# Performance work log

Measured on AMD Instinct MI355X. Metric: run time of the kernel, lower is better.

## Reference

```python
import jax, jax.numpy as jnp
import numpy as np

N_NODES = 10000
N_EDGES = 160000
B = 128
HEADS = 4
DIMS = [36, 128, 256, 512]
NEG_SLOPE = 0.2  # PyG GATConv default


def setup_inputs() -> dict:
    key = jax.random.key(0)
    ks = jax.random.split(key, 32)
    inp = {}
    inp["x"] = jax.random.normal(ks[0], (N_NODES, DIMS[0]), jnp.float32)
    inp["edge_index"] = jax.random.randint(ks[1], (2, N_EDGES), 0, N_NODES)
    inp["batch"] = jnp.sort(jax.random.randint(ks[2], (N_NODES,), 0, B))
    ki = 3
    for i in range(3):
        din, dout = DIMS[i], DIMS[i + 1]
        C = dout // HEADS
        inp[f"gcn_w{i}"] = jax.random.normal(ks[ki], (din, dout), jnp.float32) * (din ** -0.5); ki += 1
        inp[f"gcn_b{i}"] = jnp.zeros((dout,), jnp.float32)
        inp[f"gat_w{i}"] = jax.random.normal(ks[ki], (dout, dout), jnp.float32) * (dout ** -0.5); ki += 1
        inp[f"gat_as{i}"] = jax.random.normal(ks[ki], (HEADS, C), jnp.float32) * 0.1; ki += 1
        inp[f"gat_ad{i}"] = jax.random.normal(ks[ki], (HEADS, C), jnp.float32) * 0.1; ki += 1
        inp[f"gat_b{i}"] = jnp.zeros((dout,), jnp.float32)
    D = DIMS[-1]
    inp["ap_w1"] = jax.random.normal(ks[ki], (D, D // 2), jnp.float32) * (D ** -0.5); ki += 1
    inp["ap_b1"] = jnp.zeros((D // 2,), jnp.float32)
    inp["ap_w2"] = jax.random.normal(ks[ki], (D // 2, 1), jnp.float32) * ((D // 2) ** -0.5); ki += 1
    inp["ap_b2"] = jnp.zeros((1,), jnp.float32)
    return inp


def _gcn(x, w, b, src, dst, n):
    # PyG GCNConv: add self-loops, symmetric deg^-1/2 normalization, bias after agg
    h = x @ w  # [N, dout]
    deg = jax.ops.segment_sum(jnp.ones_like(dst, dtype=h.dtype), dst, n) + 1.0  # incl. self-loop
    dinv = deg ** -0.5
    norm = dinv[src] * dinv[dst]  # [E]
    agg = jax.ops.segment_sum(h[src] * norm[:, None], dst, n)
    agg = agg + h * (dinv * dinv)[:, None]  # self-loop messages
    return agg + b


def _gat(x, w, a_s, a_d, b, src, dst, n):
    # PyG GATConv: self-loops, leaky-relu logits, segment softmax over dst, concat heads
    C = w.shape[1] // HEADS
    h = (x @ w).reshape(n, HEADS, C)
    alpha_src = (h * a_s).sum(-1)  # [N, H]
    alpha_dst = (h * a_d).sum(-1)  # [N, H]
    loop = jnp.arange(n)
    s = jnp.concatenate([src, loop])
    d = jnp.concatenate([dst, loop])
    e = jax.nn.leaky_relu(alpha_src[s] + alpha_dst[d], NEG_SLOPE)  # [E+N, H]
    m = jax.ops.segment_max(e, d, n)
    ex = jnp.exp(e - m[d])
    den = jax.ops.segment_sum(ex, d, n)
    alpha = ex / den[d]  # [E+N, H]
    out = jax.ops.segment_sum(h[s] * alpha[:, :, None], d, n)  # [N, H, C]
    return out.reshape(n, HEADS * C) + b


def _forward(x, edge_index, batch, params, ap_w1, ap_b1, ap_w2, ap_b2):
    src, dst = edge_index[0], edge_index[1]
    n = x.shape[0]
    x_in = x
    n_layers = len(params)
    for i, (gw, gb, aw, a_s, a_d, ab) in enumerate(params):
        h = jax.nn.relu(_gcn(x, gw, gb, src, dst, n))  # dropout is identity in eval
        x = h + _gat(h, aw, a_s, a_d, ab, src, dst, n)
        if i < n_layers - 1:
            if x.shape[-1] == x_in.shape[-1]:
                x = x + x_in
            x_in = x
    # attention pooling (global softmax then per-graph masked renorm)
    a = jnp.tanh(x @ ap_w1 + ap_b1) @ ap_w2 + ap_b2  # [N, 1]
    a = jax.nn.softmax(a, axis=0)
    mask = jax.nn.one_hot(batch, B, dtype=x.dtype)  # [N, B]
    aw_ = a * mask
    aw_ = aw_ / (aw_.sum(0, keepdims=True) + 1e-8)
    graph_emb = aw_.T @ x  # [B, D]
    cnt = jax.ops.segment_sum(jnp.ones((n,), x.dtype), batch, B)
    ssum = jax.ops.segment_sum(x, batch, B)
    mean = ssum / jnp.maximum(cnt, 1.0)[:, None]
    smax = jax.ops.segment_max(x, batch, B)
    return jnp.concatenate([graph_emb, mean, smax, ssum], axis=1)  # [B, 4*D]


def reference(x, edge_index, batch,
              gcn_w0, gcn_b0, gat_w0, gat_as0, gat_ad0, gat_b0,
              gcn_w1, gcn_b1, gat_w1, gat_as1, gat_ad1, gat_b1,
              gcn_w2, gcn_b2, gat_w2, gat_as2, gat_ad2, gat_b2,
              ap_w1, ap_b1, ap_w2, ap_b2):
    params = [
        (gcn_w0, gcn_b0, gat_w0, gat_as0, gat_ad0, gat_b0),
        (gcn_w1, gcn_b1, gat_w1, gat_as1, gat_ad1, gat_b1),
        (gcn_w2, gcn_b2, gat_w2, gat_as2, gat_ad2, gat_b2),
    ]
    return _forward(x, edge_index, batch, params, ap_w1, ap_b1, ap_w2, ap_b2)
```

## Files before the change

kernel.cpp:

```cpp
#include <hip/hip_runtime.h>
#include <math.h>

#define NN 10000
#define NE 160000
#define NB 128
#define NH 4
#define DOUT 512
#define NEG 0.2f

typedef __attribute__((ext_vector_type(8))) short short8;
typedef __attribute__((ext_vector_type(4))) float f32x4;
typedef __attribute__((ext_vector_type(4))) unsigned short us4;

__device__ __forceinline__ float leakyf(float v){ return v > 0.f ? v : NEG*v; }
__device__ __forceinline__ void fma4(float4& a, const float4 v, float w){
  a.x += v.x*w; a.y += v.y*w; a.z += v.z*w; a.w += v.w*w;
}
__device__ __forceinline__ unsigned short f2bf(float f){
  unsigned int u = __float_as_uint(f);
  u += 0x7FFFu + ((u >> 16) & 1u);
  return (unsigned short)(u >> 16);
}
__device__ __forceinline__ float bf2f(unsigned short h){
  return __uint_as_float(((unsigned int)h) << 16);
}
__device__ __forceinline__ void split2(float v, unsigned short& h, unsigned short& l){
  h = f2bf(v);
  l = f2bf(v - bf2f(h));
}
__device__ __forceinline__ void store_hl(unsigned short* H, unsigned short* L,
                                         size_t base, float4 v){
  us4 h, l; unsigned short hh, ll;
  split2(v.x, hh, ll); h[0]=hh; l[0]=ll;
  split2(v.y, hh, ll); h[1]=hh; l[1]=ll;
  split2(v.z, hh, ll); h[2]=hh; l[2]=ll;
  split2(v.w, hh, ll); h[3]=hh; l[3]=ll;
  *(us4*)&H[base] = h;
  *(us4*)&L[base] = l;
}
__device__ __forceinline__ float4 load_hl(const unsigned short* __restrict__ H,
                                          const unsigned short* __restrict__ L, size_t base){
  us4 h = *(const us4*)&H[base];
  us4 l = *(const us4*)&L[base];
  return make_float4(bf2f(h[0])+bf2f(l[0]), bf2f(h[1])+bf2f(l[1]),
                     bf2f(h[2])+bf2f(l[2]), bf2f(h[3])+bf2f(l[3]));
}
__device__ __forceinline__ void gl_lds16(const unsigned short* g, unsigned short* l){
  __builtin_amdgcn_global_load_lds(
      (const __attribute__((address_space(1))) unsigned int*)g,
      (__attribute__((address_space(3))) unsigned int*)l, 16, 0, 0);
}

__global__ void k_count(const int* __restrict__ dst, int* __restrict__ cnt){
  int e = blockIdx.x*blockDim.x + threadIdx.x;
  if (e < NE) atomicAdd(&cnt[dst[e]], 1);
}
__global__ void k_scan(const int* __restrict__ cnt, int* __restrict__ rowptr,
                       float* __restrict__ dinv, int* __restrict__ cursor,
                       const int* __restrict__ batch, int* __restrict__ starts){
  __shared__ int part[256];
  const int CH = (NN + 255) / 256;
  int t = threadIdx.x;
  int base = t * CH;
  int s = 0;
  for (int i = 0; i < CH; i++){ int idx = base + i; if (idx < NN) s += cnt[idx]; }
  part[t] = s; __syncthreads();
  for (int o = 1; o < 256; o <<= 1){
    int v = 0;
    if (t >= o) v = part[t - o];
    __syncthreads();
    if (t >= o) part[t] += v;
    __syncthreads();
  }
  int pre = (t == 0) ? 0 : part[t - 1];
  for (int i = 0; i < CH; i++){
    int idx = base + i;
    if (idx < NN){
      int c = cnt[idx];
      rowptr[idx] = pre; pre += c;
      dinv[idx] = rsqrtf((float)c + 1.f);
      cursor[idx] = 0;
    }
  }
  if (t == 255) rowptr[NN] = part[255];
  if (t <= NB){
    int lo = 0, hi = NN;
    while (lo < hi){ int mid = (lo + hi) >> 1; if (batch[mid] < t) lo = mid + 1; else hi = mid; }
    starts[t] = lo;
  }
}
__global__ void k_fill(const int* __restrict__ src, const int* __restrict__ dst,
                       const int* __restrict__ rowptr, int* __restrict__ cursor,
                       int* __restrict__ colidx){
  int e = blockIdx.x*blockDim.x + threadIdx.x;
  if (e >= NE) return;
  int d = dst[e];
  int pos = atomicAdd(&cursor[d], 1);
  colidx[rowptr[d] + pos] = src[e];
}

struct AllConv {
  const float* src[8];
  unsigned short* dh[8];
  unsigned short* dl[8];
  int K[8], Mm[8], Kp[8], tot[8];
};
__global__ void k_convall(AllConv a){
  int j = blockIdx.y;
  int idx = blockIdx.x*blockDim.x + threadIdx.x;
  if (idx >= a.tot[j]) return;
  float v;
  if (j == 0){
    int n = idx >> 6, c = idx & 63;
    v = (c < 36) ? a.src[0][n*36 + c] : 0.f;
  } else {
    int Kp = a.Kp[j], K = a.K[j], M = a.Mm[j];
    int kk = idx % Kp, m = idx / Kp;
    v = (kk < K) ? a.src[j][(size_t)kk*M + m] : 0.f;
  }
  unsigned short h, l; split2(v, h, l);
  a.dh[j][idx] = h; a.dl[j][idx] = l;
}

#define GBM 64
#define GBN 128
#define GBK 32
__global__ __launch_bounds__(256) void k_gemm_bf3(
    const unsigned short* __restrict__ Ah, const unsigned short* __restrict__ Al,
    const unsigned short* __restrict__ Bh, const unsigned short* __restrict__ Bl,
    float* __restrict__ C, int N, int Kp, int M, int mode,
    const float* __restrict__ bias, unsigned short* __restrict__ outH,
    unsigned short* __restrict__ outL,
    const float* __restrict__ a_s, const float* __restrict__ a_d,
    float* __restrict__ as_o, float* __restrict__ ad_o, int Cdim){
  __shared__ unsigned short AsH[GBM*GBK], AsL[GBM*GBK];
  __shared__ unsigned short BsH[GBN*GBK], BsL[GBN*GBK];
  __shared__ float sred[2][GBM][4];
  int gx = M / GBN;
  int gy = (N + GBM - 1) / GBM;
  const int G = 8;
  int bid = blockIdx.x;
  int full = gy / G;
  int bid_full = full * G * gx;
  int by, bx;
  if (bid < bid_full){
    int g = bid / (G*gx); int rem = bid % (G*gx);
    by = g*G + rem % G; bx = rem / G;
  } else {
    int rem = bid - bid_full; int rows = gy - full*G;
    by = full*G + rem % rows; bx = rem / rows;
  }
  int row0 = by * GBM, col0 = bx * GBN;
  int t = threadIdx.x;
  int w = t >> 6, L = t & 63;
  int lm = L & 15, lq = L >> 4;
  int wc = w * 32;

  int sr = L >> 2, sc = L & 3;
  int art = w*16 + sr;
  int ga  = (sc - ((art >> 1) & 3)) & 3;
  int agrow = min(row0 + art, N-1);
  int brt0 = w*16 + sr;
  int brt1 = (w+4)*16 + sr;
  int gb0 = (sc - ((brt0 >> 1) & 3)) & 3;
  int gb1 = (sc - ((brt1 >> 1) & 3)) & 3;
  int bgrow0 = col0 + brt0, bgrow1 = col0 + brt1;

  int rc = (lq + (lm >> 1)) & 3;
  int aoff[4], boff[2];
#pragma unroll
  for (int mi = 0; mi < 4; mi++) aoff[mi] = (mi*16 + lm)*32 + rc*8;
#pragma unroll
  for (int ni = 0; ni < 2; ni++) boff[ni] = (wc + ni*16 + lm)*32 + rc*8;

  f32x4 acc[4][2];
#pragma unroll
  for (int i = 0; i < 4; i++)
#pragma unroll
    for (int j = 0; j < 2; j++) acc[i][j] = (f32x4){0.f,0.f,0.f,0.f};

  int nk = Kp / GBK;
  for (int kt = 0; kt < nk; kt++){
    int k0 = kt * GBK;
    if (kt) __syncthreads();
    gl_lds16(&Ah[(size_t)agrow*Kp + k0 + ga*8],  &AsH[w*512]);
    gl_lds16(&Al[(size_t)agrow*Kp + k0 + ga*8],  &AsL[w*512]);
    gl_lds16(&Bh[(size_t)bgrow0*Kp + k0 + gb0*8], &BsH[w*512]);
    gl_lds16(&Bh[(size_t)bgrow1*Kp + k0 + gb1*8], &BsH[(w+4)*512]);
    gl_lds16(&Bl[(size_t)bgrow0*Kp + k0 + gb0*8], &BsL[w*512]);
    gl_lds16(&Bl[(size_t)bgrow1*Kp + k0 + gb1*8], &BsL[(w+4)*512]);
    __syncthreads();

    short8 ah[4], al[4], bh[2], bl[2];
#pragma unroll
    for (int mi = 0; mi < 4; mi++){
      ah[mi] = *(const short8*)&AsH[aoff[mi]];
      al[mi] = *(const short8*)&AsL[aoff[mi]];
    }
#pragma unroll
    for (int ni = 0; ni < 2; ni++){
      bh[ni] = *(const short8*)&BsH[boff[ni]];
      bl[ni] = *(const short8*)&BsL[boff[ni]];
    }
#pragma unroll
    for (int mi = 0; mi < 4; mi++)
#pragma unroll
      for (int ni = 0; ni < 2; ni++){
        acc[mi][ni] = __builtin_amdgcn_mfma_f32_16x16x32_bf16(ah[mi], bh[ni], acc[mi][ni], 0, 0, 0);
        acc[mi][ni] = __builtin_amdgcn_mfma_f32_16x16x32_bf16(ah[mi], bl[ni], acc[mi][ni], 0, 0, 0);
        acc[mi][ni] = __builtin_amdgcn_mfma_f32_16x16x32_bf16(al[mi], bh[ni], acc[mi][ni], 0, 0, 0);
      }
  }
  if (mode == 1){
#pragma unroll
    for (int mi = 0; mi < 4; mi++)
#pragma unroll
      for (int ni = 0; ni < 2; ni++){
#pragma unroll
        for (int r = 0; r < 4; r++){
          int row = row0 + mi*16 + lq*4 + r;
          int col = col0 + wc + ni*16 + lm;
          if (row < N){
            float v = fmaxf(acc[mi][ni][r] + bias[col], 0.f);
            unsigned short hh, ll; split2(v, hh, ll);
            outH[(size_t)row*M + col] = hh;
            outL[(size_t)row*M + col] = ll;
          }
        }
      }
  } else if (mode != 3){
#pragma unroll
    for (int mi = 0; mi < 4; mi++)
#pragma unroll
      for (int ni = 0; ni < 2; ni++){
#pragma unroll
        for (int r = 0; r < 4; r++){
          int row = row0 + mi*16 + lq*4 + r;
          int col = col0 + wc + ni*16 + lm;
          if (row < N) C[(size_t)row*M + col] = acc[mi][ni][r];
        }
      }
  }
  if (mode == 2){
    float sA0 = a_s[col0 + wc + lm], sA1 = a_s[col0 + wc + 16 + lm];
    float dA0 = a_d[col0 + wc + lm], dA1 = a_d[col0 + wc + 16 + lm];
#pragma unroll
    for (int mi = 0; mi < 4; mi++)
#pragma unroll
      for (int r = 0; r < 4; r++){
        float vs = acc[mi][0][r]*sA0 + acc[mi][1][r]*sA1;
        float vd = acc[mi][0][r]*dA0 + acc[mi][1][r]*dA1;
#pragma unroll
        for (int o = 1; o <= 8; o <<= 1){
          vs += __shfl_xor(vs, o);
          vd += __shfl_xor(vd, o);
        }
        if (lm == 0){
          int row = mi*16 + lq*4 + r;
          sred[0][row][w] = vs;
          sred[1][row][w] = vd;
        }
      }
    __syncthreads();
    if (t < GBM){
      int n = row0 + t;
      if (n < N){
        int wph = Cdim >> 5;
        int nheads = 4 / wph;
        for (int g = 0; g < nheads; g++){
          float ss = 0.f, dd = 0.f;
          for (int q = 0; q < wph; q++){
            ss += sred[0][t][g*wph + q];
            dd += sred[1][t][g*wph + q];
          }
          int hd = (col0 + g*wph*32) / Cdim;
          as_o[n*NH + hd] = ss;
          ad_o[n*NH + hd] = dd;
        }
      }
    }
  } else if (mode == 3){
    float b0 = bias[col0 + wc + lm], b1v = bias[col0 + wc + 16 + lm];
    float w0v = a_s[col0 + wc + lm], w1v = a_s[col0 + wc + 16 + lm];
#pragma unroll
    for (int mi = 0; mi < 4; mi++)
#pragma unroll
      for (int r = 0; r < 4; r++){
        float v = tanhf(acc[mi][0][r] + b0)*w0v + tanhf(acc[mi][1][r] + b1v)*w1v;
#pragma unroll
        for (int o = 1; o <= 8; o <<= 1) v += __shfl_xor(v, o);
        if (lm == 0) sred[0][mi*16 + lq*4 + r][w] = v;
      }
    __syncthreads();
    if (t < GBM){
      int n = row0 + t;
      if (n < N){
        float s = sred[0][t][0] + sred[0][t][1] + sred[0][t][2] + sred[0][t][3];
        atomicAdd(&as_o[n], s);
      }
    }
  }
}

__global__ __launch_bounds__(256) void k_gcn_pre(
    const unsigned short* __restrict__ inH, const unsigned short* __restrict__ inL,
    const float* __restrict__ dinv,
    const int* __restrict__ rowptr, const int* __restrict__ colidx,
    unsigned short* __restrict__ outH, unsigned short* __restrict__ outL,
    int Kp, int nchunk){
  int bid = blockIdx.x;
  int chunk = bid % nchunk, grp = bid / nchunk;
  int t = threadIdx.x;
  int sub = t & 15;
  int n = grp*16 + (t >> 4);
  if (n >= NN) return;
  int f0 = chunk*64 + sub*4;
  int b = rowptr[n], e = rowptr[n+1];
  float dn = dinv[n];
  float4 a0 = make_float4(0,0,0,0), a1 = make_float4(0,0,0,0);
  float4 a2 = make_float4(0,0,0,0), a3 = make_float4(0,0,0,0);
  int j = b;
  for (; j + 3 < e; j += 4){
    int s0 = colidx[j], s1 = colidx[j+1], s2 = colidx[j+2], s3 = colidx[j+3];
    float w0 = dinv[s0], w1 = dinv[s1], w2 = dinv[s2], w3 = dinv[s3];
    float4 v0 = load_hl(inH, inL, (size_t)s0*Kp + f0);
    float4 v1 = load_hl(inH, inL, (size_t)s1*Kp + f0);
    float4 v2 = load_hl(inH, inL, (size_t)s2*Kp + f0);
    float4 v3 = load_hl(inH, inL, (size_t)s3*Kp + f0);
    fma4(a0, v0, w0*dn); fma4(a1, v1, w1*dn);
    fma4(a2, v2, w2*dn); fma4(a3, v3, w3*dn);
  }
  for (; j < e; j++){
    int s = colidx[j];
    float4 v = load_hl(inH, inL, (size_t)s*Kp + f0);
    fma4(a0, v, dinv[s]*dn);
  }
  float4 acc = make_float4(a0.x+a1.x+a2.x+a3.x, a0.y+a1.y+a2.y+a3.y,
                           a0.z+a1.z+a2.z+a3.z, a0.w+a1.w+a2.w+a3.w);
  float4 sv = load_hl(inH, inL, (size_t)n*Kp + f0);
  float dn2 = dn*dn;
  acc.x += sv.x*dn2; acc.y += sv.y*dn2; acc.z += sv.z*dn2; acc.w += sv.w*dn2;
  store_hl(outH, outL, (size_t)n*Kp + f0, acc);
}

__global__ void k_gat_maxden(const int* __restrict__ rowptr, const int* __restrict__ colidx,
                             const float* __restrict__ as_, const float* __restrict__ ad_,
                             float* __restrict__ eself, float* __restrict__ den,
                             float* __restrict__ mmax, float* __restrict__ ealpha){
  int idx = blockIdx.x*blockDim.x + threadIdx.x;
  if (idx >= NN*NH) return;
  int n = idx >> 2, hd = idx & 3;
  float adn = ad_[idx];
  float selflog = leakyf(as_[idx] + adn);
  int b = rowptr[n], e = rowptr[n+1];
  float m = selflog, d = 1.f;
  int j = b;
  for (; j + 3 < e; j += 4){
    int s0 = colidx[j], s1 = colidx[j+1], s2 = colidx[j+2], s3 = colidx[j+3];
    float l0 = leakyf(as_[s0*NH + hd] + adn), l1 = leakyf(as_[s1*NH + hd] + adn);
    float l2 = leakyf(as_[s2*NH + hd] + adn), l3 = leakyf(as_[s3*NH + hd] + adn);
    ealpha[(size_t)(j+0)*NH + hd] = l0; ealpha[(size_t)(j+1)*NH + hd] = l1;
    ealpha[(size_t)(j+2)*NH + hd] = l2; ealpha[(size_t)(j+3)*NH + hd] = l3;
    float m4 = fmaxf(fmaxf(l0, l1), fmaxf(l2, l3));
    if (m4 > m){ d *= expf(m - m4); m = m4; }
    d += expf(l0 - m) + expf(l1 - m) + expf(l2 - m) + expf(l3 - m);
  }
  for (; j < e; j++){
    float l = leakyf(as_[colidx[j]*NH + hd] + adn);
    ealpha[(size_t)j*NH + hd] = l;
    if (l > m){ d *= expf(m - l); m = l; }
    d += expf(l - m);
  }
  eself[idx] = expf(selflog - m);
  den[idx] = d;
  mmax[idx] = m;
}
__global__ __launch_bounds__(256) void k_gat_gather(
    const float* __restrict__ hg,
    const unsigned short* __restrict__ inH, const unsigned short* __restrict__ inL,
    const int* __restrict__ rowptr, const int* __restrict__ colidx,
    const float* __restrict__ ealpha, const float* __restrict__ eself,
    const float* __restrict__ den, const float* __restrict__ mmax,
    const float* __restrict__ ab,
    unsigned short* __restrict__ outH, unsigned short* __restrict__ outL,
    int M, int C, int nchunk){
  int bid = blockIdx.x;
  int chunk = bid % nchunk, grp = bid / nchunk;
  int t = threadIdx.x;
  int sub = t & 15;
  int n = grp*16 + (t >> 4);
  if (n >= NN) return;
  int f0 = chunk*64 + sub*4;
  int hd = f0 / C;
  int b = rowptr[n], e = rowptr[n+1];
  int ai = n*NH + hd;
  float mm = mmax[ai];
  float4 a0 = make_float4(0,0,0,0), a1 = make_float4(0,0,0,0);
  float4 a2 = make_float4(0,0,0,0), a3 = make_float4(0,0,0,0);
  int j = b;
  for (; j + 3 < e; j += 4){
    int s0 = colidx[j], s1 = colidx[j+1], s2 = colidx[j+2], s3 = colidx[j+3];
    float e0 = expf(ealpha[(size_t)(j+0)*NH + hd] - mm);
    float e1 = expf(ealpha[(size_t)(j+1)*NH + hd] - mm);
    float e2 = expf(ealpha[(size_t)(j+2)*NH + hd] - mm);
    float e3 = expf(ealpha[(size_t)(j+3)*NH + hd] - mm);
    float4 v0 = *(const float4*)&hg[(size_t)s0*M + f0];
    float4 v1 = *(const float4*)&hg[(size_t)s1*M + f0];
    float4 v2 = *(const float4*)&hg[(size_t)s2*M + f0];
    float4 v3 = *(const float4*)&hg[(size_t)s3*M + f0];
    fma4(a0, v0, e0); fma4(a1, v1, e1);
    fma4(a2, v2, e2); fma4(a3, v3, e3);
  }
  for (; j < e; j++){
    int s = colidx[j];
    float4 v = *(const float4*)&hg[(size_t)s*M + f0];
    fma4(a0, v, expf(ealpha[(size_t)j*NH + hd] - mm));
  }
  float4 acc = make_float4(a0.x+a1.x+a2.x+a3.x, a0.y+a1.y+a2.y+a3.y,
                           a0.z+a1.z+a2.z+a3.z, a0.w+a1.w+a2.w+a3.w);
  float es = eself[ai], inv = 1.f/den[ai];
  float4 sv = *(const float4*)&hg[(size_t)n*M + f0];
  float4 hv = load_hl(inH, inL, (size_t)n*M + f0);
  float4 bb = *(const float4*)&ab[f0];
  float4 r = make_float4(
    hv.x + bb.x + (sv.x*es + acc.x)*inv,
    hv.y + bb.y + (sv.y*es + acc.y)*inv,
    hv.z + bb.z + (sv.z*es + acc.z)*inv,
    hv.w + bb.w + (sv.w*es + acc.w)*inv);
  store_hl(outH, outL, (size_t)n*M + f0, r);
}

__global__ void k_pool(const unsigned short* __restrict__ xH, const unsigned short* __restrict__ xL,
                       const float* __restrict__ apre, const int* __restrict__ starts,
                       float* __restrict__ out){
  __shared__ float red[128];
  int g = blockIdx.x, t = threadIdx.x;
  int b = starts[g], e = starts[g+1];
  float m = -INFINITY;
  for (int n = b + t; n < e; n += 128) m = fmaxf(m, apre[n]);
  red[t] = m; __syncthreads();
  for (int o = 64; o > 0; o >>= 1){
    if (t < o) red[t] = fmaxf(red[t], red[t + o]);
    __syncthreads();
  }
  m = red[0]; __syncthreads();
  float s = 0.f;
  for (int n = b + t; n < e; n += 128) s += expf(apre[n] - m);
  red[t] = s; __syncthreads();
  for (int o = 64; o > 0; o >>= 1){
    if (t < o) red[t] += red[t + o];
    __syncthreads();
  }
  float inv = 1.f / (red[0] + 1e-8f);
  float4 sum = make_float4(0,0,0,0), wacc = make_float4(0,0,0,0);
  float4 mx = make_float4(-INFINITY,-INFINITY,-INFINITY,-INFINITY);
  for (int n = b; n < e; n++){
    float4 xv = load_hl(xH, xL, (size_t)n*DOUT + t*4);
    float p = expf(apre[n] - m) * inv;
    sum.x += xv.x; sum.y += xv.y; sum.z += xv.z; sum.w += xv.w;
    mx.x = fmaxf(mx.x, xv.x); mx.y = fmaxf(mx.y, xv.y);
    mx.z = fmaxf(mx.z, xv.z); mx.w = fmaxf(mx.w, xv.w);
    fma4(wacc, xv, p);
  }
  float ic = 1.f / fmaxf((float)(e - b), 1.f);
  float4* o = (float4*)(out + (size_t)g*4*DOUT);
  o[t]       = wacc;
  o[128 + t] = make_float4(sum.x*ic, sum.y*ic, sum.z*ic, sum.w*ic);
  o[256 + t] = mx;
  o[384 + t] = sum;
}

extern "C" void kernel_launch(void* const* d_in, const int* in_sizes, int n_in,
                              void* d_out, int out_size, void* d_ws, size_t ws_size,
                              hipStream_t stream) {
  const float* x0   = (const float*)d_in[0];
  const int*   ei   = (const int*)d_in[1];
  const int*   src  = ei;
  const int*   dst  = ei + NE;
  const int*   batch= (const int*)d_in[2];
  const float* gw[3]  = {(const float*)d_in[3],  (const float*)d_in[9],  (const float*)d_in[15]};
  const float* gb[3]  = {(const float*)d_in[4],  (const float*)d_in[10], (const float*)d_in[16]};
  const float* aw[3]  = {(const float*)d_in[5],  (const float*)d_in[11], (const float*)d_in[17]};
  const float* asw[3] = {(const float*)d_in[6],  (const float*)d_in[12], (const float*)d_in[18]};
  const float* adw[3] = {(const float*)d_in[7],  (const float*)d_in[13], (const float*)d_in[19]};
  const float* ab[3]  = {(const float*)d_in[8],  (const float*)d_in[14], (const float*)d_in[20]};
  const float* apw1 = (const float*)d_in[21];
  const float* apb1 = (const float*)d_in[22];
  const float* apw2 = (const float*)d_in[23];
  float* out = (float*)d_out;

  char* p = (char*)d_ws;
  auto alloc = [&](size_t bytes) -> void* {
    void* r = (void*)p; p += (bytes + 255) & ~(size_t)255; return r;
  };
  float* f1 = (float*)alloc((size_t)NN*512*4);
  unsigned short* actH0 = (unsigned short*)alloc((size_t)NN*512*2);
  unsigned short* actL0 = (unsigned short*)alloc((size_t)NN*512*2);
  unsigned short* actH1 = (unsigned short*)alloc((size_t)NN*512*2);
  unsigned short* actL1 = (unsigned short*)alloc((size_t)NN*512*2);
  unsigned short* preH  = (unsigned short*)alloc((size_t)NN*256*2);
  unsigned short* preL  = (unsigned short*)alloc((size_t)NN*256*2);
  unsigned short* x0h = (unsigned short*)alloc((size_t)NN*64*2);
  unsigned short* x0l = (unsigned short*)alloc((size_t)NN*64*2);
  const int wK[7]  = {36, 128, 128, 256, 256, 512, 512};
  const int wM[7]  = {128, 128, 256, 256, 512, 512, 256};
  const int wKp[7] = {64, 128, 128, 256, 256, 512, 512};
  const float* wsrc[7] = {gw[0], aw[0], gw[1], aw[1], gw[2], aw[2], apw1};
  unsigned short* wTh[7]; unsigned short* wTl[7];
  for (int i = 0; i < 7; i++){
    size_t sz = (size_t)wM[i]*wKp[i]*2;
    wTh[i] = (unsigned short*)alloc(sz);
    wTl[i] = (unsigned short*)alloc(sz);
  }
  float* ealpha = (float*)alloc((size_t)NE*NH*4);
  float* dinv = (float*)alloc(NN*4);
  float* as_  = (float*)alloc(NN*NH*4);
  float* ad_  = (float*)alloc(NN*NH*4);
  float* eself= (float*)alloc(NN*NH*4);
  float* den  = (float*)alloc(NN*NH*4);
  float* mmax = (float*)alloc(NN*NH*4);
  float* apre = (float*)alloc(NN*4);
  int* rowptr = (int*)alloc((NN+1)*4);
  int* colidx = (int*)alloc((size_t)NE*4);
  int* cnt    = (int*)alloc(NN*4);
  int* cursor = (int*)alloc(NN*4);
  int* starts = (int*)alloc((NB+1)*4);

  hipMemsetAsync(cnt, 0, NN*sizeof(int), stream);
  k_count<<<(NE+255)/256, 256, 0, stream>>>(dst, cnt);
  k_scan<<<1, 256, 0, stream>>>(cnt, rowptr, dinv, cursor, batch, starts);
  k_fill<<<(NE+255)/256, 256, 0, stream>>>(src, dst, rowptr, cursor, colidx);

  AllConv ac;
  ac.src[0] = x0; ac.dh[0] = x0h; ac.dl[0] = x0l;
  ac.K[0] = 36; ac.Mm[0] = NN; ac.Kp[0] = 64; ac.tot[0] = NN*64;
  int maxtot = NN*64;
  for (int i = 0; i < 7; i++){
    ac.src[i+1] = wsrc[i]; ac.dh[i+1] = wTh[i]; ac.dl[i+1] = wTl[i];
    ac.K[i+1] = wK[i]; ac.Mm[i+1] = wM[i]; ac.Kp[i+1] = wKp[i];
    ac.tot[i+1] = wKp[i]*wM[i];
    if (ac.tot[i+1] > maxtot) maxtot = ac.tot[i+1];
  }
  k_convall<<<dim3((maxtot+255)/256, 8), 256, 0, stream>>>(ac);

  const int dims[4] = {36, 128, 256, 512};
  const int ngrp = (NN + 15) / 16;
  const unsigned short* curH = x0h; const unsigned short* curL = x0l;
  int wi = 0;
  for (int i = 0; i < 3; i++){
    int Kin = (i == 0) ? 64 : dims[i];
    int M = dims[i+1], C = M/NH;
    int nchunk_in = Kin / 64;
    int nchunk = M / 64;
    int nblk = (M/GBN) * ((NN+GBM-1)/GBM);
    k_gcn_pre<<<nchunk_in*ngrp, 256, 0, stream>>>(curH, curL, dinv, rowptr, colidx,
                                                  preH, preL, Kin, nchunk_in);
    k_gemm_bf3<<<nblk, 256, 0, stream>>>(preH, preL, wTh[wi], wTl[wi], f1, NN, wKp[wi], M,
                                         1, gb[i], actH0, actL0,
                                         nullptr, nullptr, nullptr, nullptr, C);
    wi++;
    k_gemm_bf3<<<nblk, 256, 0, stream>>>(actH0, actL0, wTh[wi], wTl[wi], f1, NN, wKp[wi], M,
                                         2, nullptr, nullptr, nullptr,
                                         asw[i], adw[i], as_, ad_, C);
    wi++;
    k_gat_maxden<<<(NN*NH+255)/256, 256, 0, stream>>>(rowptr, colidx, as_, ad_,
                                                      eself, den, mmax, ealpha);
    k_gat_gather<<<nchunk*ngrp, 256, 0, stream>>>(f1, actH0, actL0, rowptr, colidx,
                                                  ealpha, eself, den, mmax, ab[i],
                                                  actH1, actL1, M, C, nchunk);
    curH = actH1; curL = actL1;
  }

  hipMemsetAsync(apre, 0, NN*sizeof(float), stream);
  {
    int nblk = (256/GBN) * ((NN+GBM-1)/GBM);
    k_gemm_bf3<<<nblk, 256, 0, stream>>>(actH1, actL1, wTh[6], wTl[6], f1, NN, wKp[6], 256,
                                         3, apb1, nullptr, nullptr,
                                         apw2, nullptr, apre, nullptr, 64);
  }
  k_pool<<<NB, 128, 0, stream>>>(actH1, actL1, apre, starts, out);
}
```

Measured before the change: 455.9 us.

## Fuse GAT softmax max/denominator into gather with online softmax

```diff
diff --git a/kernel.cpp b/kernel.cpp
--- a/kernel.cpp
+++ b/kernel.cpp
@@ -15,6 +15,9 @@
 __device__ __forceinline__ float leakyf(float v){ return v > 0.f ? v : NEG*v; }
 __device__ __forceinline__ void fma4(float4& a, const float4 v, float w){
   a.x += v.x*w; a.y += v.y*w; a.z += v.z*w; a.w += v.w*w;
+}
+__device__ __forceinline__ void mul4(float4& a, float s){
+  a.x *= s; a.y *= s; a.z *= s; a.w *= s;
 }
 __device__ __forceinline__ unsigned short f2bf(float f){
   unsigned int u = __float_as_uint(f);
@@ -57,7 +60,8 @@
 }
 __global__ void k_scan(const int* __restrict__ cnt, int* __restrict__ rowptr,
                        float* __restrict__ dinv, int* __restrict__ cursor,
-                       const int* __restrict__ batch, int* __restrict__ starts){
+                       const int* __restrict__ batch, int* __restrict__ starts,
+                       float* __restrict__ apre){
   __shared__ int part[256];
   const int CH = (NN + 255) / 256;
   int t = threadIdx.x;
@@ -80,6 +84,7 @@
       rowptr[idx] = pre; pre += c;
       dinv[idx] = rsqrtf((float)c + 1.f);
       cursor[idx] = 0;
+      apre[idx] = 0.f;
     }
   }
   if (t == 255) rowptr[NN] = part[255];
@@ -343,44 +348,11 @@
   store_hl(outH, outL, (size_t)n*Kp + f0, acc);
 }
 
-__global__ void k_gat_maxden(const int* __restrict__ rowptr, const int* __restrict__ colidx,
-                             const float* __restrict__ as_, const float* __restrict__ ad_,
-                             float* __restrict__ eself, float* __restrict__ den,
-                             float* __restrict__ mmax, float* __restrict__ ealpha){
-  int idx = blockIdx.x*blockDim.x + threadIdx.x;
-  if (idx >= NN*NH) return;
-  int n = idx >> 2, hd = idx & 3;
-  float adn = ad_[idx];
-  float selflog = leakyf(as_[idx] + adn);
-  int b = rowptr[n], e = rowptr[n+1];
-  float m = selflog, d = 1.f;
-  int j = b;
-  for (; j + 3 < e; j += 4){
-    int s0 = colidx[j], s1 = colidx[j+1], s2 = colidx[j+2], s3 = colidx[j+3];
-    float l0 = leakyf(as_[s0*NH + hd] + adn), l1 = leakyf(as_[s1*NH + hd] + adn);
-    float l2 = leakyf(as_[s2*NH + hd] + adn), l3 = leakyf(as_[s3*NH + hd] + adn);
-    ealpha[(size_t)(j+0)*NH + hd] = l0; ealpha[(size_t)(j+1)*NH + hd] = l1;
-    ealpha[(size_t)(j+2)*NH + hd] = l2; ealpha[(size_t)(j+3)*NH + hd] = l3;
-    float m4 = fmaxf(fmaxf(l0, l1), fmaxf(l2, l3));
-    if (m4 > m){ d *= expf(m - m4); m = m4; }
-    d += expf(l0 - m) + expf(l1 - m) + expf(l2 - m) + expf(l3 - m);
-  }
-  for (; j < e; j++){
-    float l = leakyf(as_[colidx[j]*NH + hd] + adn);
-    ealpha[(size_t)j*NH + hd] = l;
-    if (l > m){ d *= expf(m - l); m = l; }
-    d += expf(l - m);
-  }
-  eself[idx] = expf(selflog - m);
-  den[idx] = d;
-  mmax[idx] = m;
-}
 __global__ __launch_bounds__(256) void k_gat_gather(
     const float* __restrict__ hg,
     const unsigned short* __restrict__ inH, const unsigned short* __restrict__ inL,
     const int* __restrict__ rowptr, const int* __restrict__ colidx,
-    const float* __restrict__ ealpha, const float* __restrict__ eself,
-    const float* __restrict__ den, const float* __restrict__ mmax,
+    const float* __restrict__ as_, const float* __restrict__ ad_,
     const float* __restrict__ ab,
     unsigned short* __restrict__ outH, unsigned short* __restrict__ outL,
     int M, int C, int nchunk){
@@ -394,31 +366,48 @@
   int hd = f0 / C;
   int b = rowptr[n], e = rowptr[n+1];
   int ai = n*NH + hd;
-  float mm = mmax[ai];
+  float adn = ad_[ai];
+  float selflog = leakyf(as_[ai] + adn);
+  float m = selflog, d = 1.f;
   float4 a0 = make_float4(0,0,0,0), a1 = make_float4(0,0,0,0);
   float4 a2 = make_float4(0,0,0,0), a3 = make_float4(0,0,0,0);
   int j = b;
   for (; j + 3 < e; j += 4){
     int s0 = colidx[j], s1 = colidx[j+1], s2 = colidx[j+2], s3 = colidx[j+3];
-    float e0 = expf(ealpha[(size_t)(j+0)*NH + hd] - mm);
-    float e1 = expf(ealpha[(size_t)(j+1)*NH + hd] - mm);
-    float e2 = expf(ealpha[(size_t)(j+2)*NH + hd] - mm);
-    float e3 = expf(ealpha[(size_t)(j+3)*NH + hd] - mm);
+    float l0 = leakyf(as_[s0*NH + hd] + adn), l1 = leakyf(as_[s1*NH + hd] + adn);
+    float l2 = leakyf(as_[s2*NH + hd] + adn), l3 = leakyf(as_[s3*NH + hd] + adn);
     float4 v0 = *(const float4*)&hg[(size_t)s0*M + f0];
     float4 v1 = *(const float4*)&hg[(size_t)s1*M + f0];
     float4 v2 = *(const float4*)&hg[(size_t)s2*M + f0];
     float4 v3 = *(const float4*)&hg[(size_t)s3*M + f0];
-    fma4(a0, v0, e0); fma4(a1, v1, e1);
-    fma4(a2, v2, e2); fma4(a3, v3, e3);
+    float m4 = fmaxf(fmaxf(l0, l1), fmaxf(l2, l3));
+    if (m4 > m){
+      float sc = expf(m - m4);
+      d *= sc; mul4(a0, sc); mul4(a1, sc); mul4(a2, sc); mul4(a3, sc);
+      m = m4;
+    }
+    float w0 = expf(l0 - m), w1 = expf(l1 - m);
+    float w2 = expf(l2 - m), w3 = expf(l3 - m);
+    d += (w0 + w1) + (w2 + w3);
+    fma4(a0, v0, w0); fma4(a1, v1, w1);
+    fma4(a2, v2, w2); fma4(a3, v3, w3);
   }
   for (; j < e; j++){
     int s = colidx[j];
+    float l = leakyf(as_[s*NH + hd] + adn);
     float4 v = *(const float4*)&hg[(size_t)s*M + f0];
-    fma4(a0, v, expf(ealpha[(size_t)j*NH + hd] - mm));
+    if (l > m){
+      float sc = expf(m - l);
+      d *= sc; mul4(a0, sc); mul4(a1, sc); mul4(a2, sc); mul4(a3, sc);
+      m = l;
+    }
+    float ww = expf(l - m);
+    d += ww;
+    fma4(a0, v, ww);
   }
   float4 acc = make_float4(a0.x+a1.x+a2.x+a3.x, a0.y+a1.y+a2.y+a3.y,
                            a0.z+a1.z+a2.z+a3.z, a0.w+a1.w+a2.w+a3.w);
-  float es = eself[ai], inv = 1.f/den[ai];
+  float es = expf(selflog - m), inv = 1.f/d;
   float4 sv = *(const float4*)&hg[(size_t)n*M + f0];
   float4 hv = load_hl(inH, inL, (size_t)n*M + f0);
   float4 bb = *(const float4*)&ab[f0];
@@ -512,13 +501,9 @@
     wTh[i] = (unsigned short*)alloc(sz);
     wTl[i] = (unsigned short*)alloc(sz);
   }
-  float* ealpha = (float*)alloc((size_t)NE*NH*4);
   float* dinv = (float*)alloc(NN*4);
   float* as_  = (float*)alloc(NN*NH*4);
   float* ad_  = (float*)alloc(NN*NH*4);
-  float* eself= (float*)alloc(NN*NH*4);
-  float* den  = (float*)alloc(NN*NH*4);
-  float* mmax = (float*)alloc(NN*NH*4);
   float* apre = (float*)alloc(NN*4);
   int* rowptr = (int*)alloc((NN+1)*4);
   int* colidx = (int*)alloc((size_t)NE*4);
@@ -528,7 +513,7 @@
 
   hipMemsetAsync(cnt, 0, NN*sizeof(int), stream);
   k_count<<<(NE+255)/256, 256, 0, stream>>>(dst, cnt);
-  k_scan<<<1, 256, 0, stream>>>(cnt, rowptr, dinv, cursor, batch, starts);
+  k_scan<<<1, 256, 0, stream>>>(cnt, rowptr, dinv, cursor, batch, starts, apre);
   k_fill<<<(NE+255)/256, 256, 0, stream>>>(src, dst, rowptr, cursor, colidx);
 
   AllConv ac;
@@ -563,15 +548,12 @@
                                          2, nullptr, nullptr, nullptr,
                                          asw[i], adw[i], as_, ad_, C);
     wi++;
-    k_gat_maxden<<<(NN*NH+255)/256, 256, 0, stream>>>(rowptr, colidx, as_, ad_,
-                                                      eself, den, mmax, ealpha);
     k_gat_gather<<<nchunk*ngrp, 256, 0, stream>>>(f1, actH0, actL0, rowptr, colidx,
-                                                  ealpha, eself, den, mmax, ab[i],
+                                                  as_, ad_, ab[i],
                                                   actH1, actL1, M, C, nchunk);
     curH = actH1; curL = actL1;
   }
 
-  hipMemsetAsync(apre, 0, NN*sizeof(float), stream);
   {
     int nblk = (256/GBN) * ((NN+GBM-1)/GBM);
     k_gemm_bf3<<<nblk, 256, 0, stream>>>(actH1, actL1, wTh[6], wTl[6], f1, NN, wKp[6], 256,
```

Result: faster. 441.5 us (-3.2%).
